# Kernel tuning notes

Hardware: AMD Instinct MI355X
Metric: run time of the kernel (lower is better)

## Reference

```python
import jax, jax.numpy as jnp
import numpy as np

N = 2_000_000   # samples
V = 16          # num_variables
L = 4           # num_layers -> 2^(L-1) = 8 leaves; internal levels of size 1,2,4


def setup_inputs() -> dict:
    key = jax.random.key(0)
    ks = jax.random.split(key, 12)
    return {
        "x": jax.random.normal(ks[0], (N, V), dtype=jnp.float32),
        "W_leaf": jax.random.normal(ks[1], (8, V), dtype=jnp.float32),
        "b_leaf": jax.random.normal(ks[2], (8,), dtype=jnp.float32),
        "w0": jax.random.normal(ks[3], (1,), dtype=jnp.float32),
        "w1": jax.random.normal(ks[4], (2,), dtype=jnp.float32),
        "w2": jax.random.normal(ks[5], (4,), dtype=jnp.float32),
        "b0": jax.random.normal(ks[6], (1,), dtype=jnp.float32),
        "b1": jax.random.normal(ks[7], (2,), dtype=jnp.float32),
        "b2": jax.random.normal(ks[8], (4,), dtype=jnp.float32),
        "om0": jax.random.normal(ks[9], (1, 4), dtype=jnp.float32),
        "om1": jax.random.normal(ks[10], (2, 4), dtype=jnp.float32),
        "om2": jax.random.normal(ks[11], (4, 4), dtype=jnp.float32),
    }


def _combine(h, w, b, om):
    # h: [N, 2n] hidden values of children (even=left, odd=right, heap order)
    l = h[:, 0::2]            # [N, n]
    r = h[:, 1::2]            # [N, n]
    s = l + r
    sm = jax.nn.softmax(om, axis=-1)          # [n, 4] over ops ['+','*','sin','id']
    # operator_p: p = [l+r, l*r, sin(l+r), l+r]; 'id' op is also l+r in the source
    val = sm[:, 0] * s + sm[:, 1] * (l * r) + sm[:, 2] * jnp.sin(s) + sm[:, 3] * s
    return w * val + b        # [N, n]


def reference(x, W_leaf, b_leaf, w0, w1, w2, b0, b1, b2, om0, om1, om2):
    # Leaves (layer L-1): h_j = <W_leaf[j], x> + b_leaf[j]
    h = x @ W_leaf.T + b_leaf                 # [N, 8]
    # Reduce the complete binary tree bottom-up: levels of 4, 2, 1 internal nodes.
    for w, b, om in ((w2, b2, om2), (w1, b1, om1), (w0, b0, om0)):
        h = _combine(h, w, b, om)
    return h[:, 0]                            # [N] = y_hat per sample
```

## Files before the change

kernel.cpp:

```cpp
#include <hip/hip_runtime.h>
#include <math.h>


__global__ __launch_bounds__(256) void tree_rnn_kernel(
    const float* __restrict__ x,
    const float* __restrict__ W_leaf,
    const float* __restrict__ b_leaf,
    const float* __restrict__ w0,
    const float* __restrict__ w1,
    const float* __restrict__ w2,
    const float* __restrict__ b0,
    const float* __restrict__ b1,
    const float* __restrict__ b2,
    const float* __restrict__ om0,
    const float* __restrict__ om1,
    const float* __restrict__ om2,
    float* __restrict__ out,
    int n)
{
    float W[8][16];
#pragma unroll
    for (int j = 0; j < 8; ++j)
#pragma unroll
        for (int v = 0; v < 16; ++v)
            W[j][v] = W_leaf[j * 16 + v];

    float bl[8];
#pragma unroll
    for (int j = 0; j < 8; ++j) bl[j] = b_leaf[j];

    float A2[4], B2[4], C2[4], D2[4];
#pragma unroll
    for (int j = 0; j < 4; ++j) {
        float o0 = om2[j * 4 + 0], o1 = om2[j * 4 + 1];
        float o2 = om2[j * 4 + 2], o3 = om2[j * 4 + 3];
        float m  = fmaxf(fmaxf(o0, o1), fmaxf(o2, o3));
        float e0 = expf(o0 - m), e1 = expf(o1 - m);
        float e2 = expf(o2 - m), e3 = expf(o3 - m);
        float inv = 1.0f / (e0 + e1 + e2 + e3);
        float wj = w2[j];
        A2[j] = wj * (e0 + e3) * inv;
        B2[j] = wj * e1 * inv;
        C2[j] = wj * e2 * inv;
        D2[j] = b2[j];
    }
    float A1[2], B1[2], C1[2], D1[2];
#pragma unroll
    for (int j = 0; j < 2; ++j) {
        float o0 = om1[j * 4 + 0], o1 = om1[j * 4 + 1];
        float o2 = om1[j * 4 + 2], o3 = om1[j * 4 + 3];
        float m  = fmaxf(fmaxf(o0, o1), fmaxf(o2, o3));
        float e0 = expf(o0 - m), e1 = expf(o1 - m);
        float e2 = expf(o2 - m), e3 = expf(o3 - m);
        float inv = 1.0f / (e0 + e1 + e2 + e3);
        float wj = w1[j];
        A1[j] = wj * (e0 + e3) * inv;
        B1[j] = wj * e1 * inv;
        C1[j] = wj * e2 * inv;
        D1[j] = b1[j];
    }
    float A0, B0, C0, D0;
    {
        float o0 = om0[0], o1 = om0[1], o2 = om0[2], o3 = om0[3];
        float m  = fmaxf(fmaxf(o0, o1), fmaxf(o2, o3));
        float e0 = expf(o0 - m), e1 = expf(o1 - m);
        float e2 = expf(o2 - m), e3 = expf(o3 - m);
        float inv = 1.0f / (e0 + e1 + e2 + e3);
        float wj = w0[0];
        A0 = wj * (e0 + e3) * inv;
        B0 = wj * e1 * inv;
        C0 = wj * e2 * inv;
        D0 = b0[0];
    }

    const long long stride = (long long)gridDim.x * blockDim.x;
    for (long long i = (long long)blockIdx.x * blockDim.x + threadIdx.x;
         i < n; i += stride) {
        const float4* xr = reinterpret_cast<const float4*>(x) + i * 4;
        float4 va = xr[0];
        float4 vb = xr[1];
        float4 vc = xr[2];
        float4 vd = xr[3];
        float xv[16] = {va.x, va.y, va.z, va.w,
                        vb.x, vb.y, vb.z, vb.w,
                        vc.x, vc.y, vc.z, vc.w,
                        vd.x, vd.y, vd.z, vd.w};

        float h[8];
#pragma unroll
        for (int j = 0; j < 8; ++j) {
            float acc = bl[j];
#pragma unroll
            for (int v = 0; v < 16; ++v)
                acc = fmaf(xv[v], W[j][v], acc);
            h[j] = acc;
        }

        float g4[4];
#pragma unroll
        for (int j = 0; j < 4; ++j) {
            float l = h[2 * j], r = h[2 * j + 1];
            float s = l + r;
            g4[j] = fmaf(A2[j], s,
                     fmaf(B2[j], l * r,
                      fmaf(C2[j], sinf(s), D2[j])));
        }

        float g2[2];
#pragma unroll
        for (int j = 0; j < 2; ++j) {
            float l = g4[2 * j], r = g4[2 * j + 1];
            float s = l + r;
            g2[j] = fmaf(A1[j], s,
                     fmaf(B1[j], l * r,
                      fmaf(C1[j], sinf(s), D1[j])));
        }

        {
            float l = g2[0], r = g2[1];
            float s = l + r;
            float o = fmaf(A0, s,
                       fmaf(B0, l * r,
                        fmaf(C0, sinf(s), D0)));
            out[i] = o;
        }
    }
}

extern "C" void kernel_launch(void* const* d_in, const int* in_sizes, int n_in,
                              void* d_out, int out_size, void* d_ws, size_t ws_size,
                              hipStream_t stream) {
    const float* x      = (const float*)d_in[0];
    const float* W_leaf = (const float*)d_in[1];
    const float* b_leaf = (const float*)d_in[2];
    const float* w0     = (const float*)d_in[3];
    const float* w1     = (const float*)d_in[4];
    const float* w2     = (const float*)d_in[5];
    const float* b0     = (const float*)d_in[6];
    const float* b1     = (const float*)d_in[7];
    const float* b2     = (const float*)d_in[8];
    const float* om0    = (const float*)d_in[9];
    const float* om1    = (const float*)d_in[10];
    const float* om2    = (const float*)d_in[11];
    float* out = (float*)d_out;

    int n = in_sizes[0] / 16;
    int block = 256;
    int grid = 2048;
    if (grid > (n + block - 1) / block) grid = (n + block - 1) / block;

    tree_rnn_kernel<<<grid, block, 0, stream>>>(
        x, W_leaf, b_leaf, w0, w1, w2, b0, b1, b2, om0, om1, om2, out, n);
}
```

Baseline: 211.0 us.

## Precompute softmax coefficients in a prep kernel and use one thread per sample

Moves the per-thread softmax and coefficient setup into a single-thread prep kernel that writes the folded coefficients to the workspace. The main kernel reads them through uniform (scalar) loads. The grid-stride loop is replaced by a grid with one thread per sample, and W_leaf is read directly instead of being preloaded into registers. This removes redundant per-thread exp and divide setup and lowers register pressure, at the cost of an extra serial kernel launch and many more blocks.

```diff
diff --git a/kernel.cpp b/kernel.cpp
--- a/kernel.cpp
+++ b/kernel.cpp
@@ -2,128 +2,108 @@
 #include <math.h>
 
 
+__global__ void prep_kernel(
+    const float* __restrict__ b_leaf,
+    const float* __restrict__ w0, const float* __restrict__ w1,
+    const float* __restrict__ w2,
+    const float* __restrict__ b0, const float* __restrict__ b1,
+    const float* __restrict__ b2,
+    const float* __restrict__ om0, const float* __restrict__ om1,
+    const float* __restrict__ om2,
+    float* __restrict__ ws)
+{
+    for (int j = 0; j < 4; ++j) {
+        float o0 = om2[j*4+0], o1 = om2[j*4+1], o2 = om2[j*4+2], o3 = om2[j*4+3];
+        float m  = fmaxf(fmaxf(o0, o1), fmaxf(o2, o3));
+        float e0 = expf(o0-m), e1 = expf(o1-m), e2 = expf(o2-m), e3 = expf(o3-m);
+        float inv = 1.0f / (e0+e1+e2+e3);
+        float wj = w2[j];
+        ws[0+j]  = wj * (e0+e3) * inv;
+        ws[4+j]  = wj * e1 * inv;
+        ws[8+j]  = wj * e2 * inv;
+        ws[12+j] = b2[j];
+    }
+    for (int j = 0; j < 2; ++j) {
+        float o0 = om1[j*4+0], o1 = om1[j*4+1], o2 = om1[j*4+2], o3 = om1[j*4+3];
+        float m  = fmaxf(fmaxf(o0, o1), fmaxf(o2, o3));
+        float e0 = expf(o0-m), e1 = expf(o1-m), e2 = expf(o2-m), e3 = expf(o3-m);
+        float inv = 1.0f / (e0+e1+e2+e3);
+        float wj = w1[j];
+        ws[16+j] = wj * (e0+e3) * inv;
+        ws[18+j] = wj * e1 * inv;
+        ws[20+j] = wj * e2 * inv;
+        ws[22+j] = b1[j];
+    }
+    {
+        float o0 = om0[0], o1 = om0[1], o2 = om0[2], o3 = om0[3];
+        float m  = fmaxf(fmaxf(o0, o1), fmaxf(o2, o3));
+        float e0 = expf(o0-m), e1 = expf(o1-m), e2 = expf(o2-m), e3 = expf(o3-m);
+        float inv = 1.0f / (e0+e1+e2+e3);
+        float wj = w0[0];
+        ws[24] = wj * (e0+e3) * inv;
+        ws[25] = wj * e1 * inv;
+        ws[26] = wj * e2 * inv;
+        ws[27] = b0[0];
+    }
+    for (int j = 0; j < 8; ++j) ws[28+j] = b_leaf[j];
+}
+
 __global__ __launch_bounds__(256) void tree_rnn_kernel(
     const float* __restrict__ x,
     const float* __restrict__ W_leaf,
-    const float* __restrict__ b_leaf,
-    const float* __restrict__ w0,
-    const float* __restrict__ w1,
-    const float* __restrict__ w2,
-    const float* __restrict__ b0,
-    const float* __restrict__ b1,
-    const float* __restrict__ b2,
-    const float* __restrict__ om0,
-    const float* __restrict__ om1,
-    const float* __restrict__ om2,
+    const float* __restrict__ coef,
     float* __restrict__ out,
     int n)
 {
-    float W[8][16];
+    int i = blockIdx.x * 256 + threadIdx.x;
+    if (i >= n) return;
+
+    const float4* xr = reinterpret_cast<const float4*>(x) + (long long)i * 4;
+    float4 va = xr[0];
+    float4 vb = xr[1];
+    float4 vc = xr[2];
+    float4 vd = xr[3];
+    float xv[16] = {va.x, va.y, va.z, va.w,
+                    vb.x, vb.y, vb.z, vb.w,
+                    vc.x, vc.y, vc.z, vc.w,
+                    vd.x, vd.y, vd.z, vd.w};
+
+    float h[8];
 #pragma unroll
-    for (int j = 0; j < 8; ++j)
+    for (int j = 0; j < 8; ++j) {
+        float acc = coef[28 + j];
 #pragma unroll
         for (int v = 0; v < 16; ++v)
-            W[j][v] = W_leaf[j * 16 + v];
+            acc = fmaf(xv[v], W_leaf[j * 16 + v], acc);
+        h[j] = acc;
+    }
 
-    float bl[8];
-#pragma unroll
-    for (int j = 0; j < 8; ++j) bl[j] = b_leaf[j];
-
-    float A2[4], B2[4], C2[4], D2[4];
+    float g4[4];
 #pragma unroll
     for (int j = 0; j < 4; ++j) {
-        float o0 = om2[j * 4 + 0], o1 = om2[j * 4 + 1];
-        float o2 = om2[j * 4 + 2], o3 = om2[j * 4 + 3];
-        float m  = fmaxf(fmaxf(o0, o1), fmaxf(o2, o3));
-        float e0 = expf(o0 - m), e1 = expf(o1 - m);
-        float e2 = expf(o2 - m), e3 = expf(o3 - m);
-        float inv = 1.0f / (e0 + e1 + e2 + e3);
-        float wj = w2[j];
-        A2[j] = wj * (e0 + e3) * inv;
-        B2[j] = wj * e1 * inv;
-        C2[j] = wj * e2 * inv;
-        D2[j] = b2[j];
+        float l = h[2*j], r = h[2*j+1];
+        float s = l + r;
+        g4[j] = fmaf(coef[0+j], s,
+                 fmaf(coef[4+j], l * r,
+                  fmaf(coef[8+j], sinf(s), coef[12+j])));
     }
-    float A1[2], B1[2], C1[2], D1[2];
+
+    float g2[2];
 #pragma unroll
     for (int j = 0; j < 2; ++j) {
-        float o0 = om1[j * 4 + 0], o1 = om1[j * 4 + 1];
-        float o2 = om1[j * 4 + 2], o3 = om1[j * 4 + 3];
-        float m  = fmaxf(fmaxf(o0, o1), fmaxf(o2, o3));
-        float e0 = expf(o0 - m), e1 = expf(o1 - m);
-        float e2 = expf(o2 - m), e3 = expf(o3 - m);
-        float inv = 1.0f / (e0 + e1 + e2 + e3);
-        float wj = w1[j];
-        A1[j] = wj * (e0 + e3) * inv;
-        B1[j] = wj * e1 * inv;
-        C1[j] = wj * e2 * inv;
-        D1[j] = b1[j];
-    }
-    float A0, B0, C0, D0;
-    {
-        float o0 = om0[0], o1 = om0[1], o2 = om0[2], o3 = om0[3];
-        float m  = fmaxf(fmaxf(o0, o1), fmaxf(o2, o3));
-        float e0 = expf(o0 - m), e1 = expf(o1 - m);
-        float e2 = expf(o2 - m), e3 = expf(o3 - m);
-        float inv = 1.0f / (e0 + e1 + e2 + e3);
-        float wj = w0[0];
-        A0 = wj * (e0 + e3) * inv;
-        B0 = wj * e1 * inv;
-        C0 = wj * e2 * inv;
-        D0 = b0[0];
+        float l = g4[2*j], r = g4[2*j+1];
+        float s = l + r;
+        g2[j] = fmaf(coef[16+j], s,
+                 fmaf(coef[18+j], l * r,
+                  fmaf(coef[20+j], sinf(s), coef[22+j])));
     }
 
-    const long long stride = (long long)gridDim.x * blockDim.x;
-    for (long long i = (long long)blockIdx.x * blockDim.x + threadIdx.x;
-         i < n; i += stride) {
-        const float4* xr = reinterpret_cast<const float4*>(x) + i * 4;
-        float4 va = xr[0];
-        float4 vb = xr[1];
-        float4 vc = xr[2];
-        float4 vd = xr[3];
-        float xv[16] = {va.x, va.y, va.z, va.w,
-                        vb.x, vb.y, vb.z, vb.w,
-                        vc.x, vc.y, vc.z, vc.w,
-                        vd.x, vd.y, vd.z, vd.w};
-
-        float h[8];
-#pragma unroll
-        for (int j = 0; j < 8; ++j) {
-            float acc = bl[j];
-#pragma unroll
-            for (int v = 0; v < 16; ++v)
-                acc = fmaf(xv[v], W[j][v], acc);
-            h[j] = acc;
-        }
-
-        float g4[4];
-#pragma unroll
-        for (int j = 0; j < 4; ++j) {
-            float l = h[2 * j], r = h[2 * j + 1];
-            float s = l + r;
-            g4[j] = fmaf(A2[j], s,
-                     fmaf(B2[j], l * r,
-                      fmaf(C2[j], sinf(s), D2[j])));
-        }
-
-        float g2[2];
-#pragma unroll
-        for (int j = 0; j < 2; ++j) {
-            float l = g4[2 * j], r = g4[2 * j + 1];
-            float s = l + r;
-            g2[j] = fmaf(A1[j], s,
-                     fmaf(B1[j], l * r,
-                      fmaf(C1[j], sinf(s), D1[j])));
-        }
-
-        {
-            float l = g2[0], r = g2[1];
-            float s = l + r;
-            float o = fmaf(A0, s,
-                       fmaf(B0, l * r,
-                        fmaf(C0, sinf(s), D0)));
-            out[i] = o;
-        }
+    {
+        float l = g2[0], r = g2[1];
+        float s = l + r;
+        out[i] = fmaf(coef[24], s,
+                  fmaf(coef[25], l * r,
+                   fmaf(coef[26], sinf(s), coef[27])));
     }
 }
 
@@ -142,13 +122,15 @@
     const float* om0    = (const float*)d_in[9];
     const float* om1    = (const float*)d_in[10];
     const float* om2    = (const float*)d_in[11];
-    float* out = (float*)d_out;
+    float* out  = (float*)d_out;
+    float* coef = (float*)d_ws;
 
     int n = in_sizes[0] / 16;
+
+    prep_kernel<<<1, 1, 0, stream>>>(b_leaf, w0, w1, w2, b0, b1, b2,
+                                     om0, om1, om2, coef);
+
     int block = 256;
-    int grid = 2048;
-    if (grid > (n + block - 1) / block) grid = (n + block - 1) / block;
-
-    tree_rnn_kernel<<<grid, block, 0, stream>>>(
-        x, W_leaf, b_leaf, w0, w1, w2, b0, b1, b2, om0, om1, om2, out, n);
+    int grid = (n + block - 1) / block;
+    tree_rnn_kernel<<<grid, block, 0, stream>>>(x, W_leaf, coef, out, n);
 }
```

Result: faster. 206.4 us (-2.2%).
